# Kernel tuning notes

Hardware: AMD Instinct MI355X
Metric: run time of the kernel (lower is better)

Reference implementation:

```python
import jax, jax.numpy as jnp
import numpy as np

GAMMA = 0.5
NUM_ITER = 5


def setup_inputs() -> dict:
    key = jax.random.key(0)
    k1, k2 = jax.random.split(key)
    V, L = 10242, 42
    def_idxs = jax.random.uniform(k1, (V, L), dtype=jnp.float32, minval=1e-4, maxval=1.0)
    def_cont_ico_crf = jax.random.normal(k2, (V, 3), dtype=jnp.float32)
    # learned parameters, initialized as in the module
    filter_weights = jnp.ones((V, V), dtype=jnp.float32)
    spatial_weights = 4.0 * jnp.eye(V, dtype=jnp.float32)
    comp_matrix = jnp.eye(L, dtype=jnp.float32)
    return {
        "def_idxs": def_idxs,
        "def_cont_ico_crf": def_cont_ico_crf,
        "filter_weights": filter_weights,
        "spatial_weights": spatial_weights,
        "comp_matrix": comp_matrix,
    }


def reference(def_idxs, def_cont_ico_crf, filter_weights, spatial_weights, comp_matrix):
    V = def_cont_ico_crf.shape[0]
    # pairwise squared L2 distances between control points: [V, V]
    sq = jnp.sum(def_cont_ico_crf * def_cont_ico_crf, axis=1)
    d2 = sq[:, None] + sq[None, :] - 2.0 * (def_cont_ico_crf @ def_cont_ico_crf.T)
    smooth_filter = jnp.exp(-d2 / (2.0 * GAMMA ** 2))
    idx = jnp.arange(V)
    smooth_filter = smooth_filter.at[idx, idx].set(0.0)  # fill_diagonal_(0)

    U = jnp.log(jnp.clip(def_idxs, 1e-06, 1.0))  # unary potentials [V, L]
    q = jax.nn.softmax(U, axis=1)
    filter_mat = filter_weights * smooth_filter

    for _ in range(NUM_ITER):
        phi_t = filter_mat @ q                      # message passing [V, L]
        phi = -(spatial_weights @ phi_t)            # spatial reweighting
        phi = phi @ comp_matrix                     # label compatibility
        q = jax.nn.softmax(U - phi, axis=1)
    return q
```

## Files before the change

### kernel.cpp

```cpp
#include <hip/hip_runtime.h>
#include <stdint.h>

#define Vn 10242
#define Ln 42
#define LPn 48
#define VPn 10496
#define RBn 41
#define JPAD 10368
#define NITER 5
#define SCL 1.69864360f
#define BR 128

typedef float4 f4;
typedef short bf16x8 __attribute__((ext_vector_type(8)));
typedef float f32x4 __attribute__((ext_vector_type(4)));

__device__ __forceinline__ unsigned cvtpk_bf16(float a, float b) {
    unsigned r;
    asm("v_cvt_pk_bf16_f32 %0, %1, %2" : "=v"(r) : "v"(a), "v"(b));
    return r;
}
__device__ __forceinline__ unsigned short f2bf_rne(float f) {
    unsigned u = __float_as_uint(f);
    u = (u + 0x7fffu + ((u >> 16) & 1u)) >> 16;
    return (unsigned short)u;
}
__device__ __forceinline__ float bf2f(unsigned short h) {
    return __uint_as_float(((unsigned)h) << 16);
}

__global__ __launch_bounds__(256) void k_detect(const float* __restrict__ F,
                                                const float* __restrict__ S,
                                                int* flags, float* __restrict__ diagS) {
    int jj = blockIdx.x * 256 + threadIdx.x;
    if (jj >= Vn / 2) return;
    int j = jj * 2;
    const float c0 = F[0];
    int violF = 0, violS = 0;
    for (int i = blockIdx.y; i < Vn; i += (int)gridDim.y) {
        size_t off = (size_t)i * Vn + j;
        float2 f = *(const float2*)(F + off);
        float2 s = *(const float2*)(S + off);
        violF |= (f.x != c0) | (f.y != c0);
        if (i == j)          { diagS[j] = s.x;     violS |= (s.y != 0.0f); }
        else if (i == j + 1) { diagS[j + 1] = s.y; violS |= (s.x != 0.0f); }
        else                 violS |= (s.x != 0.0f) | (s.y != 0.0f);
    }
    if (violF) atomicOr(&flags[0], 1);
    if (violS) atomicOr(&flags[1], 1);
}

__global__ void k_detC(const float* __restrict__ Cm, int* flags) {
    int viol = 0;
    for (int idx = threadIdx.x; idx < Ln * Ln; idx += 256) {
        int r = idx / Ln, c = idx - r * Ln;
        float expct = (r == c) ? 1.0f : 0.0f;
        viol |= (Cm[idx] != expct);
    }
    if (viol) atomicOr(&flags[3], 1);
}

__global__ __launch_bounds__(256) void k_initU(const float* __restrict__ didx,
                                               const float* __restrict__ coords,
                                               float* __restrict__ U, float* __restrict__ qA,
                                               float* __restrict__ qB,
                                               unsigned short* __restrict__ qTAh,
                                               unsigned short* __restrict__ qTAl,
                                               unsigned short* __restrict__ qTBh,
                                               unsigned short* __restrict__ qTBl,
                                               float* __restrict__ xyz) {
    int row = blockIdx.x * 256 + threadIdx.x;
    if (row >= Vn) {
        #pragma unroll
        for (int l = 0; l < LPn; ++l) {
            U[(size_t)row * LPn + l] = 0.0f;
            qA[(size_t)row * LPn + l] = 0.0f;
            qB[(size_t)row * LPn + l] = 0.0f;
            qTAh[(size_t)l * VPn + row] = 0;
            qTAl[(size_t)l * VPn + row] = 0;
            qTBh[(size_t)l * VPn + row] = 0;
            qTBl[(size_t)l * VPn + row] = 0;
        }
        *(f4*)(xyz + (size_t)row * 4) = make_float4(0.f, 0.f, 0.f, 0.f);
        return;
    }
    float ux = SCL * coords[(size_t)row * 3 + 0];
    float uy = SCL * coords[(size_t)row * 3 + 1];
    float uz = SCL * coords[(size_t)row * 3 + 2];
    float ss = ux * ux + uy * uy + uz * uz;
    *(f4*)(xyz + (size_t)row * 4) = make_float4(ux, uy, uz, ss);
    float u[Ln];
    float mx = -3.0e38f;
    #pragma unroll
    for (int l = 0; l < Ln; ++l) {
        float x = didx[(size_t)row * Ln + l];
        x = fminf(fmaxf(x, 1e-6f), 1.0f);
        u[l] = __logf(x);
        mx = fmaxf(mx, u[l]);
    }
    float s = 0.0f;
    float e[Ln];
    #pragma unroll
    for (int l = 0; l < Ln; ++l) { e[l] = __expf(u[l] - mx); s += e[l]; }
    float inv = 1.0f / s;
    #pragma unroll
    for (int l = 0; l < Ln; ++l) {
        float qv = e[l] * inv;
        unsigned short h = f2bf_rne(qv);
        U[(size_t)row * LPn + l] = u[l];
        qA[(size_t)row * LPn + l] = qv;
        qTAh[(size_t)l * VPn + row] = h;
        qTAl[(size_t)l * VPn + row] = f2bf_rne(qv - bf2f(h));
    }
    #pragma unroll
    for (int l = Ln; l < LPn; ++l) {
        U[(size_t)row * LPn + l] = 0.0f;
        qA[(size_t)row * LPn + l] = 0.0f;
        qB[(size_t)row * LPn + l] = 0.0f;
        qTAh[(size_t)l * VPn + row] = 0;
        qTAl[(size_t)l * VPn + row] = 0;
        qTBh[(size_t)l * VPn + row] = 0;
        qTBl[(size_t)l * VPn + row] = 0;
    }
}

union ShPhi {
    struct {
        uint4 Ah[8][BR];
        uint4 Al[8][BR];
        uint4 Bh[LPn][8];
        uint4 Bl[LPn][8];
    } f;
    float w[256][33];
};

template <int USEG>
__device__ __forceinline__ void mat_gen_body(const float* __restrict__ W,
                                             const float* __restrict__ X,
                                             const float* __restrict__ xyz,
                                             float* __restrict__ part, int jchunk,
                                             ShPhi& sh) {
    int t = threadIdx.x;
    int row = blockIdx.x * 256 + t;
    bool act = (row < Vn);
    int j0 = blockIdx.y * jchunk;
    int j1 = j0 + jchunk; if (j1 > Vn) j1 = Vn;
    f4 xi = make_float4(0.f, 0.f, 0.f, 0.f);
    if (USEG && act) xi = *(const f4*)(xyz + (size_t)row * 4);
    f4 acc[12];
    #pragma unroll
    for (int c = 0; c < 12; ++c) acc[c] = make_float4(0.f, 0.f, 0.f, 0.f);
    for (int jt = j0; jt < j1; jt += 32) {
        __syncthreads();
        #pragma unroll
        for (int k = 0; k < 8; ++k) {
            int idx = t + k * 256;
            int r = idx >> 3;
            int cc = (idx & 7) << 2;
            int rr = blockIdx.x * 256 + r;
            int jc = jt + cc;
            float v0 = 0.f, v1 = 0.f, v2 = 0.f, v3 = 0.f;
            if (rr < Vn) {
                const float* wp = W + (size_t)rr * Vn + jc;
                if (jc + 0 < Vn) v0 = wp[0];
                if (jc + 1 < Vn) v1 = wp[1];
                if (jc + 2 < Vn) v2 = wp[2];
                if (jc + 3 < Vn) v3 = wp[3];
            }
            sh.w[r][cc + 0] = v0; sh.w[r][cc + 1] = v1;
            sh.w[r][cc + 2] = v2; sh.w[r][cc + 3] = v3;
        }
        __syncthreads();
        int jend = j1 - jt; if (jend > 32) jend = 32;
        for (int jj = 0; jj < jend; ++jj) {
            int j = jt + jj;
            float f = sh.w[t][jj];
            if (USEG) {
                f4 xj = *(const f4*)(xyz + (size_t)j * 4);
                float dx = xi.x - xj.x, dy = xi.y - xj.y, dz = xi.z - xj.z;
                float t2 = dx * dx; t2 = fmaf(dy, dy, t2); t2 = fmaf(dz, dz, t2);
                float w = exp2f(-t2);
                w = (j == row) ? 0.0f : w;
                f *= w;
            }
            const f4* qr = (const f4*)(X + (size_t)j * LPn);
            #pragma unroll
            for (int c = 0; c < 12; ++c) {
                f4 qv = qr[c];
                acc[c].x = fmaf(f, qv.x, acc[c].x);
                acc[c].y = fmaf(f, qv.y, acc[c].y);
                acc[c].z = fmaf(f, qv.z, acc[c].z);
                acc[c].w = fmaf(f, qv.w, acc[c].w);
            }
        }
    }
    size_t base = (size_t)blockIdx.y * LPn * VPn + row;
    if (act) {
        #pragma unroll
        for (int c = 0; c < 12; ++c) {
            part[base + (size_t)(4 * c + 0) * VPn] = acc[c].x;
            part[base + (size_t)(4 * c + 1) * VPn] = acc[c].y;
            part[base + (size_t)(4 * c + 2) * VPn] = acc[c].z;
            part[base + (size_t)(4 * c + 3) * VPn] = acc[c].w;
        }
    } else if (row < VPn) {
        #pragma unroll
        for (int c = 0; c < LPn; ++c) part[base + (size_t)c * VPn] = 0.0f;
    }
}

__global__ __launch_bounds__(256, 3) void k_phi(const unsigned short* __restrict__ qTh,
                                                const unsigned short* __restrict__ qTl,
                                                const f4* __restrict__ xyz4,
                                                const float* __restrict__ Fw,
                                                const float* __restrict__ q,
                                                float* __restrict__ part,
                                                const int* __restrict__ flags,
                                                int jchunkF, int jchunkG) {
    __shared__ ShPhi sh;
    if (flags[0]) {
        if (blockIdx.x >= RBn) return;
        mat_gen_body<1>(Fw, q, (const float*)xyz4, part, jchunkG, sh);
        return;
    }
    const int t = threadIdx.x;
    const int lane = t & 63;
    const int wv = t >> 6;
    const int lo16 = lane & 15, hi4 = lane >> 4;
    const int rowbase = blockIdx.x * BR;
    f4 p0 = xyz4[rowbase + lane];
    f4 p1 = xyz4[rowbase + lane + 64];
    const float v0x = 2.f * p0.x, v0y = 2.f * p0.y, v0z = 2.f * p0.z, ns0 = -p0.w;
    const float v1x = 2.f * p1.x, v1y = 2.f * p1.y, v1z = 2.f * p1.z, ns1 = -p1.w;
    f32x4 acc[2][3];
    #pragma unroll
    for (int rs = 0; rs < 2; ++rs)
        #pragma unroll
        for (int cs = 0; cs < 3; ++cs) acc[rs][cs] = (f32x4){0.f, 0.f, 0.f, 0.f};
    const int j0 = blockIdx.y * jchunkF;
    int j1 = j0 + jchunkF; if (j1 > JPAD) j1 = JPAD;
    const int n0 = t >> 3, sl0 = t & 7;
    const int s1 = t + 256;
    const int n1 = s1 >> 3, sl1 = s1 & 7;
    const bool has1 = (s1 < LPn * 8);
    for (int jt = j0; jt < j1; jt += 64) {
        uint4 bh0 = *(const uint4*)(qTh + (size_t)n0 * VPn + jt + sl0 * 8);
        uint4 bl0 = *(const uint4*)(qTl + (size_t)n0 * VPn + jt + sl0 * 8);
        uint4 bh1, bl1;
        if (has1) {
            bh1 = *(const uint4*)(qTh + (size_t)n1 * VPn + jt + sl1 * 8);
            bl1 = *(const uint4*)(qTl + (size_t)n1 * VPn + jt + sl1 * 8);
        }
        const int jb = __builtin_amdgcn_readfirstlane(jt + wv * 16);
        unsigned ph0[8], ph1[8], pl0[8], pl1[8];
        #pragma unroll
        for (int m = 0; m < 16; m += 2) {
            f4 qa = xyz4[jb + m];
            f4 qb = xyz4[jb + m + 1];
            float wa0 = exp2f(fmaf(v0z, qa.z, fmaf(v0y, qa.y, fmaf(v0x, qa.x, ns0 - qa.w))));
            float wb0 = exp2f(fmaf(v0z, qb.z, fmaf(v0y, qb.y, fmaf(v0x, qb.x, ns0 - qb.w))));
            float wa1 = exp2f(fmaf(v1z, qa.z, fmaf(v1y, qa.y, fmaf(v1x, qa.x, ns1 - qa.w))));
            float wb1 = exp2f(fmaf(v1z, qb.z, fmaf(v1y, qb.y, fmaf(v1x, qb.x, ns1 - qb.w))));
            unsigned h0 = cvtpk_bf16(wa0, wb0);
            unsigned h1 = cvtpk_bf16(wa1, wb1);
            ph0[m >> 1] = h0;
            ph1[m >> 1] = h1;
            pl0[m >> 1] = cvtpk_bf16(wa0 - __uint_as_float(h0 << 16),
                                     wb0 - __uint_as_float(h0 & 0xffff0000u));
            pl1[m >> 1] = cvtpk_bf16(wa1 - __uint_as_float(h1 << 16),
                                     wb1 - __uint_as_float(h1 & 0xffff0000u));
        }
        __syncthreads();
        sh.f.Ah[2 * wv][lane]          = make_uint4(ph0[0], ph0[1], ph0[2], ph0[3]);
        sh.f.Ah[2 * wv + 1][lane]      = make_uint4(ph0[4], ph0[5], ph0[6], ph0[7]);
        sh.f.Ah[2 * wv][lane + 64]     = make_uint4(ph1[0], ph1[1], ph1[2], ph1[3]);
        sh.f.Ah[2 * wv + 1][lane + 64] = make_uint4(ph1[4], ph1[5], ph1[6], ph1[7]);
        sh.f.Al[2 * wv][lane]          = make_uint4(pl0[0], pl0[1], pl0[2], pl0[3]);
        sh.f.Al[2 * wv + 1][lane]      = make_uint4(pl0[4], pl0[5], pl0[6], pl0[7]);
        sh.f.Al[2 * wv][lane + 64]     = make_uint4(pl1[0], pl1[1], pl1[2], pl1[3]);
        sh.f.Al[2 * wv + 1][lane + 64] = make_uint4(pl1[4], pl1[5], pl1[6], pl1[7]);
        sh.f.Bh[n0][sl0 ^ (n0 & 7)] = bh0;
        sh.f.Bl[n0][sl0 ^ (n0 & 7)] = bl0;
        if (has1) {
            sh.f.Bh[n1][sl1 ^ (n1 & 7)] = bh1;
            sh.f.Bl[n1][sl1 ^ (n1 & 7)] = bl1;
        }
        __syncthreads();
        #pragma unroll
        for (int kk = 0; kk < 2; ++kk) {
            bf16x8 a0h = *(bf16x8*)&sh.f.Ah[kk * 4 + hi4][wv * 32 + lo16];
            bf16x8 a1h = *(bf16x8*)&sh.f.Ah[kk * 4 + hi4][wv * 32 + 16 + lo16];
            bf16x8 a0l = *(bf16x8*)&sh.f.Al[kk * 4 + hi4][wv * 32 + lo16];
            bf16x8 a1l = *(bf16x8*)&sh.f.Al[kk * 4 + hi4][wv * 32 + 16 + lo16];
            #pragma unroll
            for (int cs = 0; cs < 3; ++cs) {
                int n = cs * 16 + lo16;
                int slot = (kk * 4 + hi4) ^ (n & 7);
                bf16x8 bh = *(bf16x8*)&sh.f.Bh[n][slot];
                bf16x8 bl = *(bf16x8*)&sh.f.Bl[n][slot];
                acc[0][cs] = __builtin_amdgcn_mfma_f32_16x16x32_bf16(a0h, bh, acc[0][cs], 0, 0, 0);
                acc[0][cs] = __builtin_amdgcn_mfma_f32_16x16x32_bf16(a0h, bl, acc[0][cs], 0, 0, 0);
                acc[0][cs] = __builtin_amdgcn_mfma_f32_16x16x32_bf16(a0l, bh, acc[0][cs], 0, 0, 0);
                acc[1][cs] = __builtin_amdgcn_mfma_f32_16x16x32_bf16(a1h, bh, acc[1][cs], 0, 0, 0);
                acc[1][cs] = __builtin_amdgcn_mfma_f32_16x16x32_bf16(a1h, bl, acc[1][cs], 0, 0, 0);
                acc[1][cs] = __builtin_amdgcn_mfma_f32_16x16x32_bf16(a1l, bh, acc[1][cs], 0, 0, 0);
            }
        }
    }
    size_t pb = (size_t)blockIdx.y * LPn * VPn;
    #pragma unroll
    for (int rs = 0; rs < 2; ++rs)
        #pragma unroll
        for (int cs = 0; cs < 3; ++cs) {
            int col = cs * 16 + lo16;
            int row = rowbase + wv * 32 + rs * 16 + hi4 * 4;
            *(f4*)(part + pb + (size_t)col * VPn + row) =
                make_float4(acc[rs][cs][0], acc[rs][cs][1], acc[rs][cs][2], acc[rs][cs][3]);
        }
}

__global__ __launch_bounds__(256) void k_sp(const float* __restrict__ Sw,
                                            const float* __restrict__ phi,
                                            float* __restrict__ part,
                                            const int* __restrict__ flags, int jchunk) {
    if (!flags[1]) return;
    __shared__ ShPhi sh;
    mat_gen_body<0>(Sw, phi, (const float*)nullptr, part, jchunk, sh);
}

__global__ __launch_bounds__(256) void k_R0(const float* __restrict__ part,
                                            const unsigned short* __restrict__ qTh,
                                            const unsigned short* __restrict__ qTl,
                                            float* __restrict__ phi,
                                            const int* __restrict__ flags,
                                            int NS, int gate) {
    if (gate && !flags[1]) return;
    int tg = blockIdx.x * 256 + threadIdx.x;
    int c = tg / (VPn / 4);
    int r4 = (tg - c * (VPn / 4)) * 4;
    f4 s = make_float4(0.f, 0.f, 0.f, 0.f);
    for (int n = 0; n < NS; ++n) {
        f4 v = *(const f4*)(part + ((size_t)n * LPn + c) * VPn + r4);
        s.x += v.x; s.y += v.y; s.z += v.z; s.w += v.w;
    }
    if (!gate && !flags[0]) {
        ushort4 h = *(const ushort4*)(qTh + (size_t)c * VPn + r4);
        ushort4 l = *(const ushort4*)(qTl + (size_t)c * VPn + r4);
        s.x -= bf2f(h.x) + bf2f(l.x);
        s.y -= bf2f(h.y) + bf2f(l.y);
        s.z -= bf2f(h.z) + bf2f(l.z);
        s.w -= bf2f(h.w) + bf2f(l.w);
    }
    phi[(size_t)(r4 + 0) * LPn + c] = s.x;
    phi[(size_t)(r4 + 1) * LPn + c] = s.y;
    phi[(size_t)(r4 + 2) * LPn + c] = s.z;
    phi[(size_t)(r4 + 3) * LPn + c] = s.w;
}

__global__ __launch_bounds__(256) void k_B(const float* __restrict__ U,
                                           const float* __restrict__ phi,
                                           const float* __restrict__ phi2,
                                           const float* __restrict__ diagS,
                                           const float* __restrict__ Cm,
                                           const float* __restrict__ Fw,
                                           const int* __restrict__ flags,
                                           float* __restrict__ qn,
                                           unsigned short* __restrict__ qTnh,
                                           unsigned short* __restrict__ qTnl,
                                           float* __restrict__ outp, int last) {
    __shared__ float ldsC[Ln][LPn];
    int t = threadIdx.x;
    if (flags[3]) {
        for (int idx = t; idx < Ln * LPn; idx += 256) {
            int m = idx / LPn, l = idx - m * LPn;
            ldsC[m][l] = (l < Ln) ? Cm[(size_t)m * Ln + l] : 0.0f;
        }
    }
    __syncthreads();
    int row = blockIdx.x * 256 + t;
    if (row >= Vn) return;
    const float* src = flags[1] ? phi2 : phi;
    float pt[LPn];
    #pragma unroll
    for (int c = 0; c < 12; ++c) {
        f4 v = *(const f4*)(src + (size_t)row * LPn + 4 * c);
        pt[4 * c + 0] = v.x; pt[4 * c + 1] = v.y;
        pt[4 * c + 2] = v.z; pt[4 * c + 3] = v.w;
    }
    float scale = (flags[0] ? 1.0f : Fw[0]) * (flags[1] ? 1.0f : diagS[row]);
    float ph[LPn];
    if (flags[3]) {
        #pragma unroll
        for (int c = 0; c < LPn; ++c) ph[c] = 0.f;
        #pragma unroll
        for (int m = 0; m < Ln; ++m) {
            float pm = pt[m];
            #pragma unroll
            for (int c = 0; c < 12; ++c) {
                f4 cv = *(const f4*)&ldsC[m][4 * c];
                ph[4 * c + 0] = fmaf(pm, cv.x, ph[4 * c + 0]);
                ph[4 * c + 1] = fmaf(pm, cv.y, ph[4 * c + 1]);
                ph[4 * c + 2] = fmaf(pm, cv.z, ph[4 * c + 2]);
                ph[4 * c + 3] = fmaf(pm, cv.w, ph[4 * c + 3]);
            }
        }
    } else {
        #pragma unroll
        for (int c = 0; c < LPn; ++c) ph[c] = pt[c];
    }
    float lg[LPn];
    #pragma unroll
    for (int c = 0; c < 12; ++c) {
        f4 uv = *(const f4*)(U + (size_t)row * LPn + 4 * c);
        lg[4 * c + 0] = uv.x + scale * ph[4 * c + 0];
        lg[4 * c + 1] = uv.y + scale * ph[4 * c + 1];
        lg[4 * c + 2] = uv.z + scale * ph[4 * c + 2];
        lg[4 * c + 3] = uv.w + scale * ph[4 * c + 3];
    }
    float mx = lg[0];
    #pragma unroll
    for (int l = 1; l < Ln; ++l) mx = fmaxf(mx, lg[l]);
    float s = 0.f;
    float e[LPn];
    #pragma unroll
    for (int l = 0; l < Ln; ++l) { e[l] = __expf(lg[l] - mx); s += e[l]; }
    #pragma unroll
    for (int l = Ln; l < LPn; ++l) e[l] = 0.f;
    float inv = 1.0f / s;
    #pragma unroll
    for (int c = 0; c < 12; ++c) {
        f4 v = make_float4(e[4 * c + 0] * inv, e[4 * c + 1] * inv,
                           e[4 * c + 2] * inv, e[4 * c + 3] * inv);
        *(f4*)(qn + (size_t)row * LPn + 4 * c) = v;
    }
    #pragma unroll
    for (int l = 0; l < Ln; ++l) {
        float qv = e[l] * inv;
        unsigned short h = f2bf_rne(qv);
        qTnh[(size_t)l * VPn + row] = h;
        qTnl[(size_t)l * VPn + row] = f2bf_rne(qv - bf2f(h));
    }
    if (last) {
        #pragma unroll
        for (int l = 0; l < Ln; ++l) outp[(size_t)row * Ln + l] = e[l] * inv;
    }
}

extern "C" void kernel_launch(void* const* d_in, const int* in_sizes, int n_in,
                              void* d_out, int out_size, void* d_ws, size_t ws_size,
                              hipStream_t stream) {
    const float* didx   = (const float*)d_in[0];
    const float* coords = (const float*)d_in[1];
    const float* Fw     = (const float*)d_in[2];
    const float* Sw     = (const float*)d_in[3];
    const float* Cm     = (const float*)d_in[4];
    float* outp = (float*)d_out;
    float* wsf = (float*)d_ws;

    int*   flags = (int*)wsf;
    float* diagS = wsf + 16;
    float* xyz   = diagS + VPn;
    float* U     = xyz + (size_t)VPn * 4;
    float* qA    = U + (size_t)VPn * LPn;
    float* qB    = qA + (size_t)VPn * LPn;
    float* phi   = qB + (size_t)VPn * LPn;
    float* phi2  = phi + (size_t)VPn * LPn;
    unsigned short* qTAh = (unsigned short*)(phi2 + (size_t)VPn * LPn);
    unsigned short* qTAl = qTAh + (size_t)LPn * VPn;
    unsigned short* qTBh = qTAl + (size_t)LPn * VPn;
    unsigned short* qTBl = qTBh + (size_t)LPn * VPn;
    float* part  = (float*)(qTBl + (size_t)LPn * VPn);

    size_t base_f = 16 + (size_t)VPn * (1 + 4) + (size_t)VPn * LPn * 5 + (size_t)VPn * LPn * 2;
    int NS = 9;
    while (NS > 1 && (base_f + (size_t)NS * LPn * VPn) * 4 > ws_size) NS--;
    int jchunkF = (((JPAD / 64) + NS - 1) / NS) * 64;
    int jchunkG = (((Vn + NS - 1) / NS) + 31) & ~31;

    hipMemsetAsync(flags, 0, 16, stream);
    hipLaunchKernelGGL(k_detect, dim3((Vn / 2 + 255) / 256, 1024), dim3(256), 0, stream,
                       Fw, Sw, flags, diagS);
    hipLaunchKernelGGL(k_detC, dim3(1), dim3(256), 0, stream, Cm, flags);
    hipLaunchKernelGGL(k_initU, dim3(RBn), dim3(256), 0, stream,
                       didx, coords, U, qA, qB, qTAh, qTAl, qTBh, qTBl, xyz);

    float* qcur = qA;  float* qnxt = qB;
    unsigned short* qThc = qTAh;  unsigned short* qTlc = qTAl;
    unsigned short* qThn = qTBh;  unsigned short* qTln = qTBl;
    for (int it = 0; it < NITER; ++it) {
        hipLaunchKernelGGL(k_phi, dim3(VPn / BR, NS), dim3(256), 0, stream,
                           qThc, qTlc, (const f4*)xyz, Fw, qcur, part, flags,
                           jchunkF, jchunkG);
        hipLaunchKernelGGL(k_R0, dim3(LPn * (VPn / 4) / 256), dim3(256), 0, stream,
                           part, qThc, qTlc, phi, flags, NS, 0);
        hipLaunchKernelGGL(k_sp, dim3(RBn, NS), dim3(256), 0, stream,
                           Sw, phi, part, flags, jchunkG);
        hipLaunchKernelGGL(k_R0, dim3(LPn * (VPn / 4) / 256), dim3(256), 0, stream,
                           part, qThc, qTlc, phi2, flags, NS, 1);
        hipLaunchKernelGGL(k_B, dim3(RBn), dim3(256), 0, stream,
                           U, phi, phi2, diagS, Cm, Fw, flags,
                           qnxt, qThn, qTln, outp, (it == NITER - 1) ? 1 : 0);
        float* tq = qcur; qcur = qnxt; qnxt = tq;
        unsigned short* th = qThc; qThc = qThn; qThn = th;
        unsigned short* tl = qTlc; qTlc = qTln; qTln = tl;
    }
}
```

Measured before the change: 589.6 us.

## Generate MFMA A-fragments in registers and shrink k_B blocks for more parallelism

New measurement: 578.1 us, median of 2. About the same (-2.0%).

```diff
diff --git a/kernel.cpp b/kernel.cpp
--- a/kernel.cpp
+++ b/kernel.cpp
@@ -14,6 +14,7 @@
 typedef float4 f4;
 typedef short bf16x8 __attribute__((ext_vector_type(8)));
 typedef float f32x4 __attribute__((ext_vector_type(4)));
+typedef unsigned u32x4 __attribute__((ext_vector_type(4)));
 
 __device__ __forceinline__ unsigned cvtpk_bf16(float a, float b) {
     unsigned r;
@@ -126,8 +127,6 @@
 
 union ShPhi {
     struct {
-        uint4 Ah[8][BR];
-        uint4 Al[8][BR];
         uint4 Bh[LPn][8];
         uint4 Bl[LPn][8];
     } f;
@@ -228,10 +227,12 @@
     const int wv = t >> 6;
     const int lo16 = lane & 15, hi4 = lane >> 4;
     const int rowbase = blockIdx.x * BR;
-    f4 p0 = xyz4[rowbase + lane];
-    f4 p1 = xyz4[rowbase + lane + 64];
-    const float v0x = 2.f * p0.x, v0y = 2.f * p0.y, v0z = 2.f * p0.z, ns0 = -p0.w;
-    const float v1x = 2.f * p1.x, v1y = 2.f * p1.y, v1z = 2.f * p1.z, ns1 = -p1.w;
+    const int i0 = rowbase + wv * 32 + lo16;
+    const int i1 = i0 + 16;
+    f4 p0 = xyz4[i0];
+    f4 p1 = xyz4[i1];
+    const float a0x = 2.f * p0.x, a0y = 2.f * p0.y, a0z = 2.f * p0.z, c0 = -p0.w;
+    const float a1x = 2.f * p1.x, a1y = 2.f * p1.y, a1z = 2.f * p1.z, c1 = -p1.w;
     f32x4 acc[2][3];
     #pragma unroll
     for (int rs = 0; rs < 2; ++rs)
@@ -251,34 +252,30 @@
             bh1 = *(const uint4*)(qTh + (size_t)n1 * VPn + jt + sl1 * 8);
             bl1 = *(const uint4*)(qTl + (size_t)n1 * VPn + jt + sl1 * 8);
         }
-        const int jb = __builtin_amdgcn_readfirstlane(jt + wv * 16);
-        unsigned ph0[8], ph1[8], pl0[8], pl1[8];
-        #pragma unroll
-        for (int m = 0; m < 16; m += 2) {
-            f4 qa = xyz4[jb + m];
-            f4 qb = xyz4[jb + m + 1];
-            float wa0 = exp2f(fmaf(v0z, qa.z, fmaf(v0y, qa.y, fmaf(v0x, qa.x, ns0 - qa.w))));
-            float wb0 = exp2f(fmaf(v0z, qb.z, fmaf(v0y, qb.y, fmaf(v0x, qb.x, ns0 - qb.w))));
-            float wa1 = exp2f(fmaf(v1z, qa.z, fmaf(v1y, qa.y, fmaf(v1x, qa.x, ns1 - qa.w))));
-            float wb1 = exp2f(fmaf(v1z, qb.z, fmaf(v1y, qb.y, fmaf(v1x, qb.x, ns1 - qb.w))));
-            unsigned h0 = cvtpk_bf16(wa0, wb0);
-            unsigned h1 = cvtpk_bf16(wa1, wb1);
-            ph0[m >> 1] = h0;
-            ph1[m >> 1] = h1;
-            pl0[m >> 1] = cvtpk_bf16(wa0 - __uint_as_float(h0 << 16),
-                                     wb0 - __uint_as_float(h0 & 0xffff0000u));
-            pl1[m >> 1] = cvtpk_bf16(wa1 - __uint_as_float(h1 << 16),
-                                     wb1 - __uint_as_float(h1 & 0xffff0000u));
+        unsigned AH[2][2][4], AL[2][2][4];
+        #pragma unroll
+        for (int kk = 0; kk < 2; ++kk) {
+            const int jb = jt + kk * 32 + hi4 * 8;
+            float w0[8], w1[8];
+            #pragma unroll
+            for (int m = 0; m < 8; ++m) {
+                f4 xj = xyz4[jb + m];
+                w0[m] = exp2f(fmaf(a0z, xj.z, fmaf(a0y, xj.y, fmaf(a0x, xj.x, c0 - xj.w))));
+                w1[m] = exp2f(fmaf(a1z, xj.z, fmaf(a1y, xj.y, fmaf(a1x, xj.x, c1 - xj.w))));
+            }
+            #pragma unroll
+            for (int m = 0; m < 4; ++m) {
+                unsigned hh0 = cvtpk_bf16(w0[2 * m], w0[2 * m + 1]);
+                unsigned hh1 = cvtpk_bf16(w1[2 * m], w1[2 * m + 1]);
+                AH[kk][0][m] = hh0;
+                AH[kk][1][m] = hh1;
+                AL[kk][0][m] = cvtpk_bf16(w0[2 * m]     - __uint_as_float(hh0 << 16),
+                                          w0[2 * m + 1] - __uint_as_float(hh0 & 0xffff0000u));
+                AL[kk][1][m] = cvtpk_bf16(w1[2 * m]     - __uint_as_float(hh1 << 16),
+                                          w1[2 * m + 1] - __uint_as_float(hh1 & 0xffff0000u));
+            }
         }
         __syncthreads();
-        sh.f.Ah[2 * wv][lane]          = make_uint4(ph0[0], ph0[1], ph0[2], ph0[3]);
-        sh.f.Ah[2 * wv + 1][lane]      = make_uint4(ph0[4], ph0[5], ph0[6], ph0[7]);
-        sh.f.Ah[2 * wv][lane + 64]     = make_uint4(ph1[0], ph1[1], ph1[2], ph1[3]);
-        sh.f.Ah[2 * wv + 1][lane + 64] = make_uint4(ph1[4], ph1[5], ph1[6], ph1[7]);
-        sh.f.Al[2 * wv][lane]          = make_uint4(pl0[0], pl0[1], pl0[2], pl0[3]);
-        sh.f.Al[2 * wv + 1][lane]      = make_uint4(pl0[4], pl0[5], pl0[6], pl0[7]);
-        sh.f.Al[2 * wv][lane + 64]     = make_uint4(pl1[0], pl1[1], pl1[2], pl1[3]);
-        sh.f.Al[2 * wv + 1][lane + 64] = make_uint4(pl1[4], pl1[5], pl1[6], pl1[7]);
         sh.f.Bh[n0][sl0 ^ (n0 & 7)] = bh0;
         sh.f.Bl[n0][sl0 ^ (n0 & 7)] = bl0;
         if (has1) {
@@ -288,22 +285,24 @@
         __syncthreads();
         #pragma unroll
         for (int kk = 0; kk < 2; ++kk) {
-            bf16x8 a0h = *(bf16x8*)&sh.f.Ah[kk * 4 + hi4][wv * 32 + lo16];
-            bf16x8 a1h = *(bf16x8*)&sh.f.Ah[kk * 4 + hi4][wv * 32 + 16 + lo16];
-            bf16x8 a0l = *(bf16x8*)&sh.f.Al[kk * 4 + hi4][wv * 32 + lo16];
-            bf16x8 a1l = *(bf16x8*)&sh.f.Al[kk * 4 + hi4][wv * 32 + 16 + lo16];
+            union Uu { u32x4 u; bf16x8 v; };
+            Uu A0h, A0l, A1h, A1l;
+            A0h.u = (u32x4){AH[kk][0][0], AH[kk][0][1], AH[kk][0][2], AH[kk][0][3]};
+            A1h.u = (u32x4){AH[kk][1][0], AH[kk][1][1], AH[kk][1][2], AH[kk][1][3]};
+            A0l.u = (u32x4){AL[kk][0][0], AL[kk][0][1], AL[kk][0][2], AL[kk][0][3]};
+            A1l.u = (u32x4){AL[kk][1][0], AL[kk][1][1], AL[kk][1][2], AL[kk][1][3]};
             #pragma unroll
             for (int cs = 0; cs < 3; ++cs) {
                 int n = cs * 16 + lo16;
                 int slot = (kk * 4 + hi4) ^ (n & 7);
                 bf16x8 bh = *(bf16x8*)&sh.f.Bh[n][slot];
                 bf16x8 bl = *(bf16x8*)&sh.f.Bl[n][slot];
-                acc[0][cs] = __builtin_amdgcn_mfma_f32_16x16x32_bf16(a0h, bh, acc[0][cs], 0, 0, 0);
-                acc[0][cs] = __builtin_amdgcn_mfma_f32_16x16x32_bf16(a0h, bl, acc[0][cs], 0, 0, 0);
-                acc[0][cs] = __builtin_amdgcn_mfma_f32_16x16x32_bf16(a0l, bh, acc[0][cs], 0, 0, 0);
-                acc[1][cs] = __builtin_amdgcn_mfma_f32_16x16x32_bf16(a1h, bh, acc[1][cs], 0, 0, 0);
-                acc[1][cs] = __builtin_amdgcn_mfma_f32_16x16x32_bf16(a1h, bl, acc[1][cs], 0, 0, 0);
-                acc[1][cs] = __builtin_amdgcn_mfma_f32_16x16x32_bf16(a1l, bh, acc[1][cs], 0, 0, 0);
+                acc[0][cs] = __builtin_amdgcn_mfma_f32_16x16x32_bf16(A0h.v, bh, acc[0][cs], 0, 0, 0);
+                acc[0][cs] = __builtin_amdgcn_mfma_f32_16x16x32_bf16(A0h.v, bl, acc[0][cs], 0, 0, 0);
+                acc[0][cs] = __builtin_amdgcn_mfma_f32_16x16x32_bf16(A0l.v, bh, acc[0][cs], 0, 0, 0);
+                acc[1][cs] = __builtin_amdgcn_mfma_f32_16x16x32_bf16(A1h.v, bh, acc[1][cs], 0, 0, 0);
+                acc[1][cs] = __builtin_amdgcn_mfma_f32_16x16x32_bf16(A1h.v, bl, acc[1][cs], 0, 0, 0);
+                acc[1][cs] = __builtin_amdgcn_mfma_f32_16x16x32_bf16(A1l.v, bh, acc[1][cs], 0, 0, 0);
             }
         }
     }
@@ -357,27 +356,27 @@
     phi[(size_t)(r4 + 3) * LPn + c] = s.w;
 }
 
-__global__ __launch_bounds__(256) void k_B(const float* __restrict__ U,
-                                           const float* __restrict__ phi,
-                                           const float* __restrict__ phi2,
-                                           const float* __restrict__ diagS,
-                                           const float* __restrict__ Cm,
-                                           const float* __restrict__ Fw,
-                                           const int* __restrict__ flags,
-                                           float* __restrict__ qn,
-                                           unsigned short* __restrict__ qTnh,
-                                           unsigned short* __restrict__ qTnl,
-                                           float* __restrict__ outp, int last) {
+__global__ __launch_bounds__(64) void k_B(const float* __restrict__ U,
+                                          const float* __restrict__ phi,
+                                          const float* __restrict__ phi2,
+                                          const float* __restrict__ diagS,
+                                          const float* __restrict__ Cm,
+                                          const float* __restrict__ Fw,
+                                          const int* __restrict__ flags,
+                                          float* __restrict__ qn,
+                                          unsigned short* __restrict__ qTnh,
+                                          unsigned short* __restrict__ qTnl,
+                                          float* __restrict__ outp, int last) {
     __shared__ float ldsC[Ln][LPn];
     int t = threadIdx.x;
     if (flags[3]) {
-        for (int idx = t; idx < Ln * LPn; idx += 256) {
+        for (int idx = t; idx < Ln * LPn; idx += 64) {
             int m = idx / LPn, l = idx - m * LPn;
             ldsC[m][l] = (l < Ln) ? Cm[(size_t)m * Ln + l] : 0.0f;
         }
     }
     __syncthreads();
-    int row = blockIdx.x * 256 + t;
+    int row = blockIdx.x * 64 + t;
     if (row >= Vn) return;
     const float* src = flags[1] ? phi2 : phi;
     float pt[LPn];
@@ -497,7 +496,7 @@
                            Sw, phi, part, flags, jchunkG);
         hipLaunchKernelGGL(k_R0, dim3(LPn * (VPn / 4) / 256), dim3(256), 0, stream,
                            part, qThc, qTlc, phi2, flags, NS, 1);
-        hipLaunchKernelGGL(k_B, dim3(RBn), dim3(256), 0, stream,
+        hipLaunchKernelGGL(k_B, dim3(VPn / 64), dim3(64), 0, stream,
                            U, phi, phi2, diagS, Cm, Fw, flags,
                            qnxt, qThn, qTln, outp, (it == NITER - 1) ? 1 : 0);
         float* tq = qcur; qcur = qnxt; qnxt = tq;
```
